# Kernel optimization log

Measured on AMD Instinct MI355X. Metric: run time of the kernel, lower is better.

## Reference

```python
import jax, jax.numpy as jnp
import numpy as np

MAX_BLUR = 20.0
MIN_BLUR = 0.5
MIN_SCALE = 0.001


def _dct_matrix(N, dtype):
    """Orthonormal DCT-II matrix C: dct(v) = C @ v (matches torch_dct norm='ortho')."""
    n = jnp.arange(N, dtype=dtype)
    k = n[:, None]
    C = jnp.cos(jnp.pi * (n[None, :] + 0.5) * k / N)
    scale = jnp.where(k == 0, jnp.sqrt(jnp.asarray(1.0 / N, dtype)), jnp.sqrt(jnp.asarray(2.0 / N, dtype)))
    return C * scale


def setup_inputs() -> dict:
    key = jax.random.key(0)
    k1, k2 = jax.random.split(key)
    x = jax.random.normal(k1, (128, 3, 256, 256), dtype=jnp.float32)
    t = jax.random.uniform(k2, (128,), dtype=jnp.float32)
    return {"x": x, "t": t}


def reference(x, t):
    dtype = x.dtype
    N = x.shape[-1]
    # frequency grid: pi * linspace(0, N-1, N) / N, squared and summed over 2D
    freqs = jnp.pi * jnp.arange(N, dtype=dtype) / N
    freq_sq = freqs[:, None] ** 2 + freqs[None, :] ** 2  # [N, N]

    # blur schedule: exp(log(min_blur)*(1-t) + log(max_blur)*t)
    sigmas = jnp.exp(np.log(MIN_BLUR) * (1.0 - t) + np.log(MAX_BLUR) * t)
    sigmas = sigmas[:, None, None, None]  # [B,1,1,1]
    tau = sigmas ** 2 / 2

    fade_freq = jnp.exp(-freq_sq * tau)  # [B,1,N,N]
    fade_freq = jnp.where(fade_freq < 0.01, jnp.zeros((), dtype), fade_freq)

    C = _dct_matrix(N, dtype)  # [N, N]
    # separable 2D DCT-II (ortho): out[k,n] = sum_{h,w} C[k,h] C[n,w] x[h,w]
    dct_x = jnp.einsum('kh,nw,bchw->bckn', C, C, x)
    blurred_dct = dct_x * (fade_freq * (1.0 - MIN_SCALE) + MIN_SCALE)
    # inverse 2D DCT (ortho): transpose matrices
    blurred_x = jnp.einsum('kh,nw,bckn->bchw', C, C, blurred_dct)
    return blurred_x.astype(dtype)
```

## Files before the change

kernel.cpp:

```cpp
#include <hip/hip_runtime.h>
#include <hip/hip_fp16.h>

typedef _Float16 f16;
typedef _Float16 f16x8 __attribute__((ext_vector_type(8)));
typedef _Float16 f16x4 __attribute__((ext_vector_type(4)));
typedef float f32x4 __attribute__((ext_vector_type(4)));

#define NSZ 256
#define NIMG 384

__device__ __forceinline__ int sw(int r, int c) {
  return r * NSZ + (c ^ ((r & 7) << 3));
}

__global__ void prep_kernel(f16* __restrict__ Cm, f16* __restrict__ CTm,
                            float* __restrict__ g, const float* __restrict__ t) {
  int k = blockIdx.x;
  int h = threadIdx.x;
  double scale = (k == 0) ? 0.0625 : 0.08838834764831844;
  double val = cos(3.14159265358979323846 * ((double)h + 0.5) * (double)k / 256.0) * scale;
  f16 vh = (f16)((float)val);
  Cm[k * NSZ + h] = vh;
  CTm[h * NSZ + k] = vh;
  if (k < 128) {
    float tb = t[k];
    float sg = expf(-0.69314718055994531f * (1.0f - tb) + 2.99573227355399099f * tb);
    float tau = 0.5f * sg * sg;
    float f = 3.14159265358979f * (float)h / 256.0f;
    g[k * NSZ + h] = expf(-f * f * tau);
  }
}

template <bool OP1_LDS>
__device__ __forceinline__ void do_gemm(const f16* L, const f16* __restrict__ T,
                                        int r0, int c0, int lrow, int lk,
                                        f32x4 (&acc)[8][4]) {
#pragma unroll
  for (int fi = 0; fi < 8; ++fi)
#pragma unroll
    for (int fj = 0; fj < 4; ++fj) {
      f32x4 z = {0.f, 0.f, 0.f, 0.f};
      acc[fi][fj] = z;
    }
  for (int ks = 0; ks < 8; ++ks) {
    int kh = ks * 32 + lk;
    f16x8 o1[8], o2[4];
#pragma unroll
    for (int fi = 0; fi < 8; ++fi) {
      int row = r0 + fi * 16 + lrow;
      if constexpr (OP1_LDS)
        o1[fi] = *(const f16x8*)&L[sw(row, kh)];
      else
        o1[fi] = *(const f16x8*)&T[row * NSZ + kh];
    }
#pragma unroll
    for (int fj = 0; fj < 4; ++fj) {
      int row = c0 + fj * 16 + lrow;
      if constexpr (OP1_LDS)
        o2[fj] = *(const f16x8*)&T[row * NSZ + kh];
      else
        o2[fj] = *(const f16x8*)&L[sw(row, kh)];
    }
#pragma unroll
    for (int fi = 0; fi < 8; ++fi)
#pragma unroll
      for (int fj = 0; fj < 4; ++fj)
        acc[fi][fj] = __builtin_amdgcn_mfma_f32_16x16x32_f16(o1[fi], o2[fj], acc[fi][fj], 0, 0, 0);
  }
}

__device__ __forceinline__ void writeT(f16* L, int r0, int c0, int lrow, int lv4,
                                       const f32x4 (&acc)[8][4]) {
#pragma unroll
  for (int fi = 0; fi < 8; ++fi) {
    int rp = r0 + fi * 16 + lv4;
#pragma unroll
    for (int fj = 0; fj < 4; ++fj) {
      int c = c0 + fj * 16 + lrow;
      f16x4 h;
      h[0] = (f16)acc[fi][fj][0];
      h[1] = (f16)acc[fi][fj][1];
      h[2] = (f16)acc[fi][fj][2];
      h[3] = (f16)acc[fi][fj][3];
      *(f16x4*)&L[sw(c, rp)] = h;
    }
  }
}

__global__ __launch_bounds__(512, 1) void fused_kernel(
    const float* __restrict__ x, float* __restrict__ out,
    const f16* __restrict__ Cm, const f16* __restrict__ CTm,
    const float* __restrict__ g) {
  __shared__ f16 L[NSZ * NSZ];

  const int img = blockIdx.x;
  const int b = img / 3;
  const float* X = x + (size_t)img * NSZ * NSZ;
  float* Y = out + (size_t)img * NSZ * NSZ;

  const int t = threadIdx.x;
  const int lane = t & 63;
  const int wave = t >> 6;
  const int wr = wave >> 2;
  const int wc = wave & 3;
  const int r0 = wr * 128;
  const int c0 = wc * 64;
  const int lrow = lane & 15;
  const int lk = (lane >> 4) * 8;
  const int lv4 = (lane >> 4) * 4;

  for (int it = 0; it < 16; ++it) {
    int gid = it * 512 + t;
    int r = gid >> 5;
    int c8 = (gid & 31) << 3;
    const float* s = X + r * NSZ + c8;
    float4 a0 = *(const float4*)s;
    float4 a1 = *(const float4*)(s + 4);
    f16x8 v;
    v[0] = (f16)a0.x; v[1] = (f16)a0.y; v[2] = (f16)a0.z; v[3] = (f16)a0.w;
    v[4] = (f16)a1.x; v[5] = (f16)a1.y; v[6] = (f16)a1.z; v[7] = (f16)a1.w;
    *(f16x8*)&L[sw(r, c8)] = v;
  }
  __syncthreads();

  f32x4 acc[8][4];

  do_gemm<true>(L, Cm, r0, c0, lrow, lk, acc);
  __syncthreads();
  writeT(L, r0, c0, lrow, lv4, acc);
  __syncthreads();

  do_gemm<false>(L, Cm, r0, c0, lrow, lk, acc);
  {
    const float* gb = g + b * NSZ;
#pragma unroll
    for (int fi = 0; fi < 8; ++fi) {
      float4 gk = *(const float4*)&gb[r0 + fi * 16 + lv4];
      float gkv[4] = {gk.x, gk.y, gk.z, gk.w};
#pragma unroll
      for (int fj = 0; fj < 4; ++fj) {
        float gn = gb[c0 + fj * 16 + lrow];
#pragma unroll
        for (int v = 0; v < 4; ++v) {
          float fade = gkv[v] * gn;
          float s = (fade < 0.01f) ? 0.001f : (fade * 0.999f + 0.001f);
          acc[fi][fj][v] *= s;
        }
      }
    }
  }
  __syncthreads();
  writeT(L, r0, c0, lrow, lv4, acc);
  __syncthreads();

  do_gemm<true>(L, CTm, r0, c0, lrow, lk, acc);
  __syncthreads();
  writeT(L, r0, c0, lrow, lv4, acc);
  __syncthreads();

  do_gemm<true>(L, CTm, r0, c0, lrow, lk, acc);
#pragma unroll
  for (int fi = 0; fi < 8; ++fi) {
    int r = r0 + fi * 16 + lv4;
#pragma unroll
    for (int fj = 0; fj < 4; ++fj) {
      int c = c0 + fj * 16 + lrow;
#pragma unroll
      for (int v = 0; v < 4; ++v)
        Y[(size_t)(r + v) * NSZ + c] = acc[fi][fj][v];
    }
  }
}

extern "C" void kernel_launch(void* const* d_in, const int* in_sizes, int n_in,
                              void* d_out, int out_size, void* d_ws, size_t ws_size,
                              hipStream_t stream) {
  const float* x = (const float*)d_in[0];
  const float* t = (const float*)d_in[1];
  float* out = (float*)d_out;

  char* ws = (char*)d_ws;
  float* g = (float*)ws;
  f16* Cm = (f16*)(ws + 131072);
  f16* CTm = (f16*)(ws + 262144);

  prep_kernel<<<256, 256, 0, stream>>>(Cm, CTm, g, t);
  fused_kernel<<<NIMG, 512, 0, stream>>>(x, out, Cm, CTm, g);
}
```

Before: 121.1 us.

## Switch to 32x32x16 MFMA with fragment-ordered DCT tables and pipelined input load

Replaces the 16x16x32 MFMA tiling with 32x32x16 MFMA tiles and stores the DCT matrices in a fragment-major layout, so each lane reads a contiguous 16-byte fragment from global memory. The first GEMM is overlapped with the input load: x is read in four double-buffered column chunks that are consumed as they arrive. It also widens the LDS swizzle to 16 rows, drops the global-A variant by reordering the stage-4 operands, and raises launch bounds to 2 blocks per CU. The 128 KiB LDS tile likely still limits occupancy to one block per CU, and the added per-chunk barriers and larger register footprint are possible costs.

```diff
diff --git a/kernel.cpp b/kernel.cpp
--- a/kernel.cpp
+++ b/kernel.cpp
@@ -4,24 +4,28 @@
 typedef _Float16 f16;
 typedef _Float16 f16x8 __attribute__((ext_vector_type(8)));
 typedef _Float16 f16x4 __attribute__((ext_vector_type(4)));
-typedef float f32x4 __attribute__((ext_vector_type(4)));
+typedef float f32x16 __attribute__((ext_vector_type(16)));
 
 #define NSZ 256
 #define NIMG 384
 
 __device__ __forceinline__ int sw(int r, int c) {
-  return r * NSZ + (c ^ ((r & 7) << 3));
-}
-
-__global__ void prep_kernel(f16* __restrict__ Cm, f16* __restrict__ CTm,
+  return r * NSZ + (c ^ ((r & 15) << 3));
+}
+
+__device__ __forceinline__ int frag_off(int r, int c) {
+  return (((((r >> 5) * 16 + (c >> 4)) << 6) + (((c >> 3) & 1) << 5) + (r & 31)) << 3) + (c & 7);
+}
+
+__global__ void prep_kernel(f16* __restrict__ Cf, f16* __restrict__ CTf,
                             float* __restrict__ g, const float* __restrict__ t) {
   int k = blockIdx.x;
   int h = threadIdx.x;
   double scale = (k == 0) ? 0.0625 : 0.08838834764831844;
   double val = cos(3.14159265358979323846 * ((double)h + 0.5) * (double)k / 256.0) * scale;
   f16 vh = (f16)((float)val);
-  Cm[k * NSZ + h] = vh;
-  CTm[h * NSZ + k] = vh;
+  Cf[frag_off(k, h)] = vh;
+  CTf[frag_off(h, k)] = vh;
   if (k < 128) {
     float tb = t[k];
     float sg = expf(-0.69314718055994531f * (1.0f - tb) + 2.99573227355399099f * tb);
@@ -31,145 +35,198 @@
   }
 }
 
-template <bool OP1_LDS>
-__device__ __forceinline__ void do_gemm(const f16* L, const f16* __restrict__ T,
-                                        int r0, int c0, int lrow, int lk,
-                                        f32x4 (&acc)[8][4]) {
-#pragma unroll
-  for (int fi = 0; fi < 8; ++fi)
-#pragma unroll
-    for (int fj = 0; fj < 4; ++fj) {
-      f32x4 z = {0.f, 0.f, 0.f, 0.f};
-      acc[fi][fj] = z;
-    }
-  for (int ks = 0; ks < 8; ++ks) {
-    int kh = ks * 32 + lk;
-    f16x8 o1[8], o2[4];
-#pragma unroll
-    for (int fi = 0; fi < 8; ++fi) {
-      int row = r0 + fi * 16 + lrow;
-      if constexpr (OP1_LDS)
-        o1[fi] = *(const f16x8*)&L[sw(row, kh)];
-      else
-        o1[fi] = *(const f16x8*)&T[row * NSZ + kh];
-    }
-#pragma unroll
-    for (int fj = 0; fj < 4; ++fj) {
-      int row = c0 + fj * 16 + lrow;
-      if constexpr (OP1_LDS)
-        o2[fj] = *(const f16x8*)&T[row * NSZ + kh];
-      else
-        o2[fj] = *(const f16x8*)&L[sw(row, kh)];
-    }
-#pragma unroll
-    for (int fi = 0; fi < 8; ++fi)
-#pragma unroll
-      for (int fj = 0; fj < 4; ++fj)
-        acc[fi][fj] = __builtin_amdgcn_mfma_f32_16x16x32_f16(o1[fi], o2[fj], acc[fi][fj], 0, 0, 0);
-  }
-}
-
-__device__ __forceinline__ void writeT(f16* L, int r0, int c0, int lrow, int lv4,
-                                       const f32x4 (&acc)[8][4]) {
-#pragma unroll
-  for (int fi = 0; fi < 8; ++fi) {
-    int rp = r0 + fi * 16 + lv4;
-#pragma unroll
-    for (int fj = 0; fj < 4; ++fj) {
-      int c = c0 + fj * 16 + lrow;
-      f16x4 h;
-      h[0] = (f16)acc[fi][fj][0];
-      h[1] = (f16)acc[fi][fj][1];
-      h[2] = (f16)acc[fi][fj][2];
-      h[3] = (f16)acc[fi][fj][3];
-      *(f16x4*)&L[sw(c, rp)] = h;
-    }
-  }
-}
-
-__global__ __launch_bounds__(512, 1) void fused_kernel(
+#define TBL_FRAG(Tf, tile, q, lane) (*(const f16x8*)&(Tf)[((((tile) * 16 + (q)) << 6) + (lane)) << 3])
+
+__device__ __forceinline__ void gemm_AL_BT(const f16* L, const f16* __restrict__ Tf,
+                                           int rbase, int tB0, int lane,
+                                           f32x16 (&acc)[4][2]) {
+  int l31 = lane & 31, kh = (lane >> 5) * 8;
+#pragma unroll 4
+  for (int q = 0; q < 16; ++q) {
+    f16x8 a[4], b[2];
+#pragma unroll
+    for (int fi = 0; fi < 4; ++fi)
+      a[fi] = *(const f16x8*)&L[sw(rbase + fi * 32 + l31, q * 16 + kh)];
+#pragma unroll
+    for (int fj = 0; fj < 2; ++fj)
+      b[fj] = TBL_FRAG(Tf, tB0 + fj, q, lane);
+#pragma unroll
+    for (int fi = 0; fi < 4; ++fi)
+#pragma unroll
+      for (int fj = 0; fj < 2; ++fj)
+        acc[fi][fj] = __builtin_amdgcn_mfma_f32_32x32x16_f16(a[fi], b[fj], acc[fi][fj], 0, 0, 0);
+  }
+}
+
+__device__ __forceinline__ void writeT(f16* L, int rbase, int cbase, int lane,
+                                       const f32x16 (&acc)[4][2]) {
+  int l31 = lane & 31, hi4 = (lane >> 5) * 4;
+#pragma unroll
+  for (int fi = 0; fi < 4; ++fi)
+#pragma unroll
+    for (int fj = 0; fj < 2; ++fj) {
+      int crow = cbase + fj * 32 + l31;
+#pragma unroll
+      for (int v2 = 0; v2 < 4; ++v2) {
+        int colbase = rbase + fi * 32 + v2 * 8 + hi4;
+        f16x4 hv;
+        hv[0] = (f16)acc[fi][fj][v2 * 4 + 0];
+        hv[1] = (f16)acc[fi][fj][v2 * 4 + 1];
+        hv[2] = (f16)acc[fi][fj][v2 * 4 + 2];
+        hv[3] = (f16)acc[fi][fj][v2 * 4 + 3];
+        *(f16x4*)&L[sw(crow, colbase)] = hv;
+      }
+    }
+}
+
+__global__ __launch_bounds__(512, 2) void fused_kernel(
     const float* __restrict__ x, float* __restrict__ out,
-    const f16* __restrict__ Cm, const f16* __restrict__ CTm,
+    const f16* __restrict__ Cf, const f16* __restrict__ CTf,
     const float* __restrict__ g) {
   __shared__ f16 L[NSZ * NSZ];
 
   const int img = blockIdx.x;
   const int b = img / 3;
-  const float* X = x + (size_t)img * NSZ * NSZ;
-  float* Y = out + (size_t)img * NSZ * NSZ;
+  const float* X = x + (size_t)img * 65536;
+  float* Y = out + (size_t)img * 65536;
 
   const int t = threadIdx.x;
   const int lane = t & 63;
   const int wave = t >> 6;
-  const int wr = wave >> 2;
-  const int wc = wave & 3;
-  const int r0 = wr * 128;
-  const int c0 = wc * 64;
-  const int lrow = lane & 15;
-  const int lk = (lane >> 4) * 8;
-  const int lv4 = (lane >> 4) * 4;
-
-  for (int it = 0; it < 16; ++it) {
-    int gid = it * 512 + t;
-    int r = gid >> 5;
-    int c8 = (gid & 31) << 3;
-    const float* s = X + r * NSZ + c8;
-    float4 a0 = *(const float4*)s;
-    float4 a1 = *(const float4*)(s + 4);
-    f16x8 v;
-    v[0] = (f16)a0.x; v[1] = (f16)a0.y; v[2] = (f16)a0.z; v[3] = (f16)a0.w;
-    v[4] = (f16)a1.x; v[5] = (f16)a1.y; v[6] = (f16)a1.z; v[7] = (f16)a1.w;
-    *(f16x8*)&L[sw(r, c8)] = v;
-  }
-  __syncthreads();
-
-  f32x4 acc[8][4];
-
-  do_gemm<true>(L, Cm, r0, c0, lrow, lk, acc);
-  __syncthreads();
-  writeT(L, r0, c0, lrow, lv4, acc);
-  __syncthreads();
-
-  do_gemm<false>(L, Cm, r0, c0, lrow, lk, acc);
+  const int r0 = (wave >> 2) * 128;
+  const int c0 = (wave & 3) * 64;
+  const int l31 = lane & 31;
+  const int kh = (lane >> 5) * 8;
+  const int hi4 = (lane >> 5) * 4;
+  const int tB0 = c0 >> 5;
+
+  f32x16 acc[4][2];
+  const f32x16 zz = {0.f, 0.f, 0.f, 0.f, 0.f, 0.f, 0.f, 0.f,
+                     0.f, 0.f, 0.f, 0.f, 0.f, 0.f, 0.f, 0.f};
+#pragma unroll
+  for (int fi = 0; fi < 4; ++fi)
+#pragma unroll
+    for (int fj = 0; fj < 2; ++fj) acc[fi][fj] = zz;
+
+  const int xr_row = t >> 1;
+  const int xr_half = (t & 1) * 32;
+  float4 xa[2][8];
+#pragma unroll
+  for (int s = 0; s < 8; ++s) xa[0][s] = *(const float4*)&X[xr_row * NSZ + xr_half + s * 4];
+
+#pragma unroll
+  for (int cw = 0; cw < 4; ++cw) {
+    int cb = cw & 1;
+    if (cw < 3) {
+#pragma unroll
+      for (int s = 0; s < 8; ++s)
+        xa[cb ^ 1][s] = *(const float4*)&X[xr_row * NSZ + (cw + 1) * 64 + xr_half + s * 4];
+    }
+#pragma unroll
+    for (int g8 = 0; g8 < 4; ++g8) {
+      float4 a0 = xa[cb][g8 * 2], a1 = xa[cb][g8 * 2 + 1];
+      f16x8 v;
+      v[0] = (f16)a0.x; v[1] = (f16)a0.y; v[2] = (f16)a0.z; v[3] = (f16)a0.w;
+      v[4] = (f16)a1.x; v[5] = (f16)a1.y; v[6] = (f16)a1.z; v[7] = (f16)a1.w;
+      *(f16x8*)&L[sw(xr_row, cw * 64 + xr_half + g8 * 8)] = v;
+    }
+    __syncthreads();
+#pragma unroll
+    for (int q4 = 0; q4 < 4; ++q4) {
+      int q = cw * 4 + q4;
+      f16x8 a[4], bfr[2];
+#pragma unroll
+      for (int fi = 0; fi < 4; ++fi)
+        a[fi] = *(const f16x8*)&L[sw(r0 + fi * 32 + l31, q * 16 + kh)];
+#pragma unroll
+      for (int fj = 0; fj < 2; ++fj)
+        bfr[fj] = TBL_FRAG(Cf, tB0 + fj, q, lane);
+#pragma unroll
+      for (int fi = 0; fi < 4; ++fi)
+#pragma unroll
+        for (int fj = 0; fj < 2; ++fj)
+          acc[fi][fj] = __builtin_amdgcn_mfma_f32_32x32x16_f16(a[fi], bfr[fj], acc[fi][fj], 0, 0, 0);
+    }
+    __syncthreads();
+  }
+  writeT(L, r0, c0, lane, acc);
+  __syncthreads();
+
+#pragma unroll
+  for (int fi = 0; fi < 4; ++fi)
+#pragma unroll
+    for (int fj = 0; fj < 2; ++fj) acc[fi][fj] = zz;
+  gemm_AL_BT(L, Cf, r0, tB0, lane, acc);
   {
     const float* gb = g + b * NSZ;
 #pragma unroll
-    for (int fi = 0; fi < 8; ++fi) {
-      float4 gk = *(const float4*)&gb[r0 + fi * 16 + lv4];
-      float gkv[4] = {gk.x, gk.y, gk.z, gk.w};
-#pragma unroll
-      for (int fj = 0; fj < 4; ++fj) {
-        float gn = gb[c0 + fj * 16 + lrow];
-#pragma unroll
-        for (int v = 0; v < 4; ++v) {
-          float fade = gkv[v] * gn;
-          float s = (fade < 0.01f) ? 0.001f : (fade * 0.999f + 0.001f);
-          acc[fi][fj][v] *= s;
+    for (int fj = 0; fj < 2; ++fj) {
+      float gk = gb[c0 + fj * 32 + l31];
+#pragma unroll
+      for (int fi = 0; fi < 4; ++fi) {
+#pragma unroll
+        for (int v2 = 0; v2 < 4; ++v2) {
+          float4 gn = *(const float4*)&gb[r0 + fi * 32 + v2 * 8 + hi4];
+          float gnv[4] = {gn.x, gn.y, gn.z, gn.w};
+#pragma unroll
+          for (int e = 0; e < 4; ++e) {
+            float fade = gk * gnv[e];
+            float s = ((fade < 0.01f) ? 0.f : fade) * 0.999f + 0.001f;
+            acc[fi][fj][v2 * 4 + e] *= s;
+          }
         }
       }
     }
   }
   __syncthreads();
-  writeT(L, r0, c0, lrow, lv4, acc);
-  __syncthreads();
-
-  do_gemm<true>(L, CTm, r0, c0, lrow, lk, acc);
-  __syncthreads();
-  writeT(L, r0, c0, lrow, lv4, acc);
-  __syncthreads();
-
-  do_gemm<true>(L, CTm, r0, c0, lrow, lk, acc);
-#pragma unroll
-  for (int fi = 0; fi < 8; ++fi) {
-    int r = r0 + fi * 16 + lv4;
-#pragma unroll
-    for (int fj = 0; fj < 4; ++fj) {
-      int c = c0 + fj * 16 + lrow;
-#pragma unroll
-      for (int v = 0; v < 4; ++v)
-        Y[(size_t)(r + v) * NSZ + c] = acc[fi][fj][v];
-    }
-  }
+  writeT(L, r0, c0, lane, acc);
+  __syncthreads();
+
+#pragma unroll
+  for (int fi = 0; fi < 4; ++fi)
+#pragma unroll
+    for (int fj = 0; fj < 2; ++fj) acc[fi][fj] = zz;
+  gemm_AL_BT(L, CTf, r0, tB0, lane, acc);
+  __syncthreads();
+  writeT(L, r0, c0, lane, acc);
+  __syncthreads();
+
+#pragma unroll
+  for (int fi = 0; fi < 4; ++fi)
+#pragma unroll
+    for (int fj = 0; fj < 2; ++fj) acc[fi][fj] = zz;
+  {
+    int tA0 = r0 >> 5;
+#pragma unroll 4
+    for (int q = 0; q < 16; ++q) {
+      f16x8 a[4], bfr[2];
+#pragma unroll
+      for (int fi = 0; fi < 4; ++fi)
+        a[fi] = TBL_FRAG(CTf, tA0 + fi, q, lane);
+#pragma unroll
+      for (int fj = 0; fj < 2; ++fj)
+        bfr[fj] = *(const f16x8*)&L[sw(c0 + fj * 32 + l31, q * 16 + kh)];
+#pragma unroll
+      for (int fi = 0; fi < 4; ++fi)
+#pragma unroll
+        for (int fj = 0; fj < 2; ++fj)
+          acc[fi][fj] = __builtin_amdgcn_mfma_f32_32x32x16_f16(a[fi], bfr[fj], acc[fi][fj], 0, 0, 0);
+    }
+  }
+#pragma unroll
+  for (int fi = 0; fi < 4; ++fi)
+#pragma unroll
+    for (int fj = 0; fj < 2; ++fj) {
+      int w = c0 + fj * 32 + l31;
+#pragma unroll
+      for (int v2 = 0; v2 < 4; ++v2) {
+#pragma unroll
+        for (int e = 0; e < 4; ++e) {
+          int h = r0 + fi * 32 + v2 * 8 + hi4 + e;
+          Y[h * NSZ + w] = acc[fi][fj][v2 * 4 + e];
+        }
+      }
+    }
 }
 
 extern "C" void kernel_launch(void* const* d_in, const int* in_sizes, int n_in,
@@ -181,9 +238,9 @@
 
   char* ws = (char*)d_ws;
   float* g = (float*)ws;
-  f16* Cm = (f16*)(ws + 131072);
-  f16* CTm = (f16*)(ws + 262144);
-
-  prep_kernel<<<256, 256, 0, stream>>>(Cm, CTm, g, t);
-  fused_kernel<<<NIMG, 512, 0, stream>>>(x, out, Cm, CTm, g);
-}
+  f16* Cf = (f16*)(ws + 131072);
+  f16* CTf = (f16*)(ws + 262144);
+
+  prep_kernel<<<256, 256, 0, stream>>>(Cf, CTf, g, t);
+  fused_kernel<<<NIMG, 512, 0, stream>>>(x, out, Cf, CTf, g);
+}
```

Measured after the change: 99.39 us. 1.22x faster.
